# Optimization experiments

Measured on AMD Instinct MI355X. Metric: run time of the kernel, lower is better.

Reference implementation:

```python
import jax, jax.numpy as jnp
import numpy as np
import math

# Model dims (see shape_source)
N_EMBD = 2048
QK_H = 128      # per-head qk dim
V_H = 128       # per-head v dim
Q_DIM = N_EMBD                 # 2048 -> 16 query heads
N_HEAD = Q_DIM // QK_H         # 16
KV_HEAD = N_HEAD // 4          # 4 (GQA)
K_DIM = KV_HEAD * QK_H         # 512
V_DIM = KV_HEAD * V_H          # 512
D_KV = K_DIM + V_DIM           # 1024, S6 channel dim
D_STATE = 16                   # S6 state size
DT_RANK = math.ceil(D_KV / 16) # 'auto' -> 64
WINDOW = 512
B, T = 1, 4096


def setup_inputs() -> dict:
    key = jax.random.key(0)
    ks = jax.random.split(key, 8)
    x = jax.random.normal(ks[0], (B, T, N_EMBD), jnp.float32)
    W_attn = jax.random.normal(ks[1], (Q_DIM + K_DIM + V_DIM, N_EMBD), jnp.float32) * 0.02
    # S6 params (canonical Mamba S6 init: A = -exp(A_log), A_log = log(1..N))
    A_log = jnp.log(jnp.arange(1, D_STATE + 1, dtype=jnp.float32))[None, :] * jnp.ones((D_KV, 1), jnp.float32)
    x_proj_w = jax.random.normal(ks[2], (DT_RANK + 2 * D_STATE, D_KV), jnp.float32) * 0.02
    dt_proj_w = jax.random.normal(ks[3], (D_KV, DT_RANK), jnp.float32) * 0.02
    dt_proj_b = jax.random.normal(ks[4], (D_KV,), jnp.float32) * 0.1
    D_param = jnp.ones((D_KV,), jnp.float32)
    W_o = jax.random.normal(ks[5], (N_EMBD, Q_DIM), jnp.float32) * 0.02
    return dict(x=x, W_attn=W_attn, A_log=A_log, x_proj_w=x_proj_w,
                dt_proj_w=dt_proj_w, dt_proj_b=dt_proj_b, D_param=D_param,
                W_o=W_o, window_size=WINDOW)


def s6_scan(u, A_log, x_proj_w, dt_proj_w, dt_proj_b, D_param):
    """Canonical S6 selective scan. u: (B, T, D) -> (B, T, D)."""
    Bb, Tt, D = u.shape
    N = A_log.shape[1]
    dt_rank = dt_proj_w.shape[1]
    x_dbl = jnp.einsum('btd,ed->bte', u, x_proj_w)          # (B,T,dt_rank+2N)
    dt, Bm, Cm = jnp.split(x_dbl, [dt_rank, dt_rank + N], axis=-1)
    delta = jax.nn.softplus(jnp.einsum('btr,dr->btd', dt, dt_proj_w) + dt_proj_b)  # (B,T,D)
    A = -jnp.exp(A_log)                                      # (D,N), negative
    dA = jnp.exp(delta[..., None] * A)                       # (B,T,D,N)
    dBu = delta[..., None] * Bm[:, :, None, :] * u[..., None]  # (B,T,D,N)

    def step(h, inp):
        dA_t, dBu_t, C_t = inp
        h = dA_t * h + dBu_t                                 # (B,D,N)
        y = jnp.einsum('bdn,bn->bd', h, C_t)
        return h, y

    h0 = jnp.zeros((Bb, D, N), u.dtype)
    _, ys = jax.lax.scan(step, h0,
                         (dA.transpose(1, 0, 2, 3), dBu.transpose(1, 0, 2, 3), Cm.transpose(1, 0, 2)))
    y = ys.transpose(1, 0, 2)                                # (B,T,D)
    return y + D_param * u


def sliding_window_attn(q, k, v, window, scale):
    """Causal sliding-window attention; query i attends to j in [i-(window-1), i].
    q: (B,T,H,dh), k/v: (B,T,Hk,dh). Blockwise with one look-back block."""
    Bb, Tt, H, dh = q.shape
    Hk = k.shape[2]
    G = H // Hk
    k = jnp.repeat(k, G, axis=2)
    v = jnp.repeat(v, G, axis=2)
    W = window
    nb = Tt // W
    # (B,H,nb,W,dh)
    qb = q.reshape(Bb, nb, W, H, dh).transpose(0, 3, 1, 2, 4)
    kb = k.reshape(Bb, nb, W, H, dh).transpose(0, 3, 1, 2, 4)
    vb = v.reshape(Bb, nb, W, H, dh).transpose(0, 3, 1, 2, 4)
    # previous block (zeros for first block)
    kprev = jnp.pad(kb, ((0, 0), (0, 0), (1, 0), (0, 0), (0, 0)))[:, :, :nb]
    vprev = jnp.pad(vb, ((0, 0), (0, 0), (1, 0), (0, 0), (0, 0)))[:, :, :nb]
    k2 = jnp.concatenate([kprev, kb], axis=3)                # (B,H,nb,2W,dh)
    v2 = jnp.concatenate([vprev, vb], axis=3)
    scores = jnp.einsum('bhwid,bhwjd->bhwij', qb * scale, k2)  # (B,H,nb,W,2W)
    i = jnp.arange(W)[:, None]
    j = jnp.arange(2 * W)[None, :]
    rel = i + W - j                                          # absolute i - j
    base_mask = (rel >= 0) & (rel <= W - 1)                  # causal & within window
    blk = jnp.arange(nb)[:, None, None]
    valid = base_mask[None] & ((j[None] >= W) | (blk > 0))   # first block: no look-back
    neg = jnp.finfo(jnp.float32).max
    scores = jnp.where(valid[None, None], scores, -neg)
    attn = jax.nn.softmax(scores.astype(jnp.float32), axis=-1).astype(q.dtype)
    out = jnp.einsum('bhwij,bhwjd->bhwid', attn, v2)         # (B,H,nb,W,dh)
    return out.transpose(0, 2, 3, 1, 4).reshape(Bb, Tt, H, dh)


def reference(x, W_attn, A_log, x_proj_w, dt_proj_w, dt_proj_b, D_param, W_o, window_size):
    Bb, Tt, C = x.shape
    qkv = jnp.einsum('btc,oc->bto', x, W_attn)
    q = qkv[..., :Q_DIM]
    kv = qkv[..., Q_DIM:]
    kv = s6_scan(kv, A_log, x_proj_w, dt_proj_w, dt_proj_b, D_param)
    k = kv[..., :K_DIM]
    v = kv[..., K_DIM:]
    q = q.reshape(Bb, Tt, N_HEAD, QK_H)
    k = k.reshape(Bb, Tt, KV_HEAD, QK_H)
    v = v.reshape(Bb, Tt, KV_HEAD, V_H)
    scale = 1.0 / math.sqrt(QK_H)
    y = sliding_window_attn(q, k, v, window_size, scale)     # (B,T,H,v_h)
    y = y.reshape(Bb, Tt, -1)
    return jnp.einsum('bto,no->btn', y, W_o)
```

## Files before the change

### kernel.cpp

```cpp
#include <hip/hip_runtime.h>
#include <hip/hip_bf16.h>

typedef __hip_bfloat16 bf16;
typedef __attribute__((ext_vector_type(8))) short bf16x8;
typedef __attribute__((ext_vector_type(4))) float f32x4;

#define T_SEQ 4096
#define NEMBD 2048
#define QKVD  3072
#define QDIM  2048
#define DKV   1024
#define KDIM  512
#define NH    16
#define DH    128
#define NST   16
#define DTR   64
#define WIN   512
#define NCHUNK 64
#define CLEN   64

__device__ inline float bf2f(bf16 x) { return __bfloat162float(x); }

struct F8 { float v[8]; };

__device__ inline F8 load_b8(const bf16* p) {
  union { uint4 q; unsigned short s[8]; } u;
  u.q = *reinterpret_cast<const uint4*>(p);
  F8 r;
#pragma unroll
  for (int i = 0; i < 8; i++) r.v[i] = __uint_as_float((unsigned)u.s[i] << 16);
  return r;
}

__device__ inline F8 load8(const void* base, size_t idx, int f32flag) {
  if (f32flag) {
    const float4* p = reinterpret_cast<const float4*>((const float*)base + idx);
    float4 a = p[0], b = p[1];
    F8 r;
    r.v[0]=a.x; r.v[1]=a.y; r.v[2]=a.z; r.v[3]=a.w;
    r.v[4]=b.x; r.v[5]=b.y; r.v[6]=b.z; r.v[7]=b.w;
    return r;
  }
  return load_b8((const bf16*)base + idx);
}

__device__ inline float load1(const void* base, size_t idx, int f32flag) {
  return f32flag ? ((const float*)base)[idx] : bf2f(((const bf16*)base)[idx]);
}

__device__ inline unsigned short f2b_bits(float f) {
  bf16 h = __float2bfloat16(f);
  union { bf16 h; unsigned short u; } c; c.h = h; return c.u;
}

__device__ inline ushort4 pack4(float a, float b, float c, float d) {
  ushort4 r; r.x = f2b_bits(a); r.y = f2b_bits(b); r.z = f2b_bits(c); r.w = f2b_bits(d);
  return r;
}

__device__ inline void gld_lds16(const void* g, void* l) {
  __builtin_amdgcn_global_load_lds(
      (const __attribute__((address_space(1))) unsigned int*)g,
      (__attribute__((address_space(3))) unsigned int*)l, 16, 0, 0);
}

__global__ void detect_dtype(const unsigned short* __restrict__ x, int* __restrict__ flag) {
  if (threadIdx.x == 0 && blockIdx.x == 0) {
    int c = 0;
    for (int i = 0; i < 128; i++) {
      float v = __uint_as_float((unsigned)x[i] << 16);
      float a = fabsf(v);
      if (a >= 1e-8f && a <= 1e4f) c++;
    }
    flag[0] = (c >= 120) ? 0 : 1;
  }
}

__global__ __launch_bounds__(256) void cvt_bf16(
    const void* __restrict__ in, const int* __restrict__ dflag,
    unsigned short* __restrict__ out, int n8)
{
  int i = blockIdx.x * 256 + threadIdx.x;
  if (i >= n8) return;
  const int f = dflag[0];
  F8 v = load8(in, (size_t)i * 8, f);
  ushort4* o = (ushort4*)(out + (size_t)i * 8);
  o[0] = pack4(v.v[0], v.v[1], v.v[2], v.v[3]);
  o[1] = pack4(v.v[4], v.v[5], v.v[6], v.v[7]);
}

__global__ __launch_bounds__(512, 2) void gemm_wide(
    const unsigned short* __restrict__ A, const unsigned short* __restrict__ B,
    int M, int N, int K, int mode,
    bf16* __restrict__ oq, bf16* __restrict__ ou, float* __restrict__ oc)
{
  __shared__ unsigned short lds[2][384 * 64];
  const int tid = threadIdx.x;
  const int wave = tid >> 6, lane = tid & 63;
  const int quad = lane >> 4, l16 = lane & 15;
  const int wm = wave >> 2, wn = wave & 3;
  const int bm = blockIdx.y * 128, bn = blockIdx.x * 256;

  const int lrow = lane >> 3;
  const int lslot = (lane & 7) ^ lrow;
  const unsigned short* Abase = A + (size_t)(bm + wave * 8 + lrow) * K + lslot * 8;
  const unsigned short* Bbase = B + (size_t)(bn + wave * 8 + lrow) * K + lslot * 8;

  const int x7 = l16 & 7;
  const int s0 = ((0 + quad) ^ x7) * 8;
  const int s1 = ((4 + quad) ^ x7) * 8;
  const int arow0 = (wm * 64 + l16) * 64;
  const int brow0 = (128 + wn * 64 + l16) * 64;

  f32x4 acc[4][4];
#pragma unroll
  for (int i = 0; i < 4; i++)
#pragma unroll
    for (int j = 0; j < 4; j++) acc[i][j] = f32x4{0.f, 0.f, 0.f, 0.f};

  const int NT = K >> 6;

  gld_lds16(Abase,                          &lds[0][(0   + wave * 8) * 64]);
  gld_lds16(Abase + (size_t)64 * K,         &lds[0][(64  + wave * 8) * 64]);
  gld_lds16(Bbase,                          &lds[0][(128 + wave * 8) * 64]);
  gld_lds16(Bbase + (size_t)64 * K,         &lds[0][(192 + wave * 8) * 64]);
  gld_lds16(Bbase + (size_t)128 * K,        &lds[0][(256 + wave * 8) * 64]);
  gld_lds16(Bbase + (size_t)192 * K,        &lds[0][(320 + wave * 8) * 64]);
  gld_lds16(Bbase + 64,                     &lds[1][(128 + wave * 8) * 64]);
  gld_lds16(Bbase + (size_t)64 * K + 64,    &lds[1][(192 + wave * 8) * 64]);
  gld_lds16(Bbase + (size_t)128 * K + 64,   &lds[1][(256 + wave * 8) * 64]);
  gld_lds16(Bbase + (size_t)192 * K + 64,   &lds[1][(320 + wave * 8) * 64]);
  asm volatile("s_waitcnt vmcnt(4)" ::: "memory");
  __builtin_amdgcn_sched_barrier(0);
  __builtin_amdgcn_s_barrier();

#define MM(m, n) \
  acc[m][n] = __builtin_amdgcn_mfma_f32_16x16x32_bf16(aF[m][0], bF[n][0], acc[m][n], 0, 0, 0); \
  acc[m][n] = __builtin_amdgcn_mfma_f32_16x16x32_bf16(aF[m][1], bF[n][1], acc[m][n], 0, 0, 0);

  for (int g = 0; g < NT; ++g) {
    const unsigned short* L = lds[g & 1];
    unsigned short* Ln = lds[(g & 1) ^ 1];
    const bool stA = (g + 1) < NT;
    const bool stB = (g + 2) < NT;
    const size_t kA = (size_t)(g + 1) * 64;
    const size_t kB = (size_t)(g + 2) * 64;

    bf16x8 aF[4][2], bF[4][2];

    aF[0][0] = *(const bf16x8*)&L[arow0 +    0 + s0];
    aF[0][1] = *(const bf16x8*)&L[arow0 +    0 + s1];
    aF[1][0] = *(const bf16x8*)&L[arow0 + 1024 + s0];
    aF[1][1] = *(const bf16x8*)&L[arow0 + 1024 + s1];
    bF[0][0] = *(const bf16x8*)&L[brow0 +    0 + s0];
    bF[0][1] = *(const bf16x8*)&L[brow0 +    0 + s1];
    bF[1][0] = *(const bf16x8*)&L[brow0 + 1024 + s0];
    bF[1][1] = *(const bf16x8*)&L[brow0 + 1024 + s1];
    if (stA) gld_lds16(Abase + kA, &Ln[(0 + wave * 8) * 64]);
    __builtin_amdgcn_s_barrier();
    __builtin_amdgcn_s_setprio(1);
    MM(0,0); MM(0,1); MM(1,0); MM(1,1);
    __builtin_amdgcn_s_setprio(0);
    __builtin_amdgcn_s_barrier();

    bF[2][0] = *(const bf16x8*)&L[brow0 + 2048 + s0];
    bF[2][1] = *(const bf16x8*)&L[brow0 + 2048 + s1];
    bF[3][0] = *(const bf16x8*)&L[brow0 + 3072 + s0];
    bF[3][1] = *(const bf16x8*)&L[brow0 + 3072 + s1];
    if (stA) gld_lds16(Abase + (size_t)64 * K + kA, &Ln[(64 + wave * 8) * 64]);
    __builtin_amdgcn_s_barrier();
    __builtin_amdgcn_s_setprio(1);
    MM(0,2); MM(0,3); MM(1,2); MM(1,3);
    __builtin_amdgcn_s_setprio(0);
    __builtin_amdgcn_s_barrier();

    aF[2][0] = *(const bf16x8*)&L[arow0 + 2048 + s0];
    aF[2][1] = *(const bf16x8*)&L[arow0 + 2048 + s1];
    aF[3][0] = *(const bf16x8*)&L[arow0 + 3072 + s0];
    aF[3][1] = *(const bf16x8*)&L[arow0 + 3072 + s1];
    if (stB) {
      gld_lds16(Bbase + kB,                  (unsigned short*)&L[(128 + wave * 8) * 64]);
      gld_lds16(Bbase + (size_t)64 * K + kB, (unsigned short*)&L[(192 + wave * 8) * 64]);
    }
    __builtin_amdgcn_s_barrier();
    __builtin_amdgcn_s_setprio(1);
    MM(2,0); MM(2,1); MM(3,0); MM(3,1);
    __builtin_amdgcn_s_setprio(0);
    __builtin_amdgcn_s_barrier();

    if (stB) {
      gld_lds16(Bbase + (size_t)128 * K + kB, (unsigned short*)&L[(256 + wave * 8) * 64]);
      gld_lds16(Bbase + (size_t)192 * K + kB, (unsigned short*)&L[(320 + wave * 8) * 64]);
    }
    __builtin_amdgcn_s_barrier();
    __builtin_amdgcn_s_setprio(1);
    MM(2,2); MM(2,3); MM(3,2); MM(3,3);
    __builtin_amdgcn_s_setprio(0);
    if (stB) { asm volatile("s_waitcnt vmcnt(4)" ::: "memory"); }
    else     { asm volatile("s_waitcnt vmcnt(0)" ::: "memory"); }
    __builtin_amdgcn_sched_barrier(0);
    __builtin_amdgcn_s_barrier();
  }
#undef MM

#pragma unroll
  for (int m = 0; m < 4; m++)
#pragma unroll
    for (int n = 0; n < 4; n++) {
      int gm0 = bm + wm * 64 + m * 16 + quad * 4;
      int gn  = bn + wn * 64 + n * 16 + l16;
#pragma unroll
      for (int r = 0; r < 4; r++) {
        int gm = gm0 + r;
        float v = acc[m][n][r];
        if (mode == 0) {
          if (gn < QDIM) oq[(size_t)gm * QDIM + gn] = __float2bfloat16(v);
          else           ou[(size_t)gm * DKV + (gn - QDIM)] = __float2bfloat16(v);
        } else {
          oc[(size_t)gm * N + gn] = v;
        }
      }
    }
}

__global__ __launch_bounds__(256) void xdbl_mfma(
    const bf16* __restrict__ u, const unsigned short* __restrict__ xpw_bf,
    float* __restrict__ xd)
{
  __shared__ unsigned short Us[64 * 32];
  __shared__ unsigned short Ws[96 * 32];
  const int tid = threadIdx.x;
  const int wave = tid >> 6, lane = tid & 63;
  const int quad = lane >> 4, l16 = lane & 15;
  const int t0 = blockIdx.x * 64;
  const unsigned short* ub = (const unsigned short*)u;

  f32x4 acc[6];
#pragma unroll
  for (int j = 0; j < 6; j++) acc[j] = f32x4{0.f, 0.f, 0.f, 0.f};

  const int urow = tid >> 2, ucol = (tid & 3) * 8;
  const int wrow0 = tid >> 2, wcol0 = (tid & 3) * 8;
  const int wrow1 = (256 + tid) >> 2;

  uint4 upre = *(const uint4*)(ub + (size_t)(t0 + urow) * DKV + ucol);
  uint4 wpre0 = *(const uint4*)(xpw_bf + (size_t)wrow0 * DKV + wcol0);
  uint4 wpre1 = (tid < 128) ? *(const uint4*)(xpw_bf + (size_t)wrow1 * DKV + wcol0)
                            : uint4{0, 0, 0, 0};

  for (int k0 = 0; k0 < DKV; k0 += 32) {
    __syncthreads();
    *(uint4*)&Us[urow * 32 + ucol] = upre;
    *(uint4*)&Ws[wrow0 * 32 + wcol0] = wpre0;
    if (tid < 128) *(uint4*)&Ws[wrow1 * 32 + wcol0] = wpre1;
    __syncthreads();

    int kn = (k0 + 32 < DKV) ? (k0 + 32) : k0;
    upre  = *(const uint4*)(ub + (size_t)(t0 + urow) * DKV + kn + ucol);
    wpre0 = *(const uint4*)(xpw_bf + (size_t)wrow0 * DKV + kn + wcol0);
    if (tid < 128) wpre1 = *(const uint4*)(xpw_bf + (size_t)wrow1 * DKV + kn + wcol0);

    bf16x8 a = *(const bf16x8*)&Us[(wave * 16 + l16) * 32 + quad * 8];
#pragma unroll
    for (int j = 0; j < 6; j++) {
      bf16x8 b = *(const bf16x8*)&Ws[(j * 16 + l16) * 32 + quad * 8];
      acc[j] = __builtin_amdgcn_mfma_f32_16x16x32_bf16(a, b, acc[j], 0, 0, 0);
    }
  }

#pragma unroll
  for (int j = 0; j < 6; j++)
#pragma unroll
    for (int r = 0; r < 4; r++) {
      int t = t0 + wave * 16 + quad * 4 + r;
      xd[(size_t)t * 96 + j * 16 + l16] = acc[j][r];
    }
}

__global__ __launch_bounds__(256) void delta_mfma(
    const float* __restrict__ xd, const unsigned short* __restrict__ dtw_bf,
    const void* __restrict__ dtb, const int* __restrict__ dflag,
    bf16* __restrict__ delta)
{
  __shared__ unsigned short Xs[64 * 72];
  __shared__ unsigned short Ws[128 * 72];
  const int tid = threadIdx.x;
  const int wave = tid >> 6, lane = tid & 63;
  const int quad = lane >> 4, l16 = lane & 15;
  const int t0 = blockIdx.y * 64, d0 = blockIdx.x * 128;

  for (int e = tid; e < 64 * 8; e += 256) {
    int row = e >> 3, c8 = (e & 7) * 8;
    const float* p = xd + (size_t)(t0 + row) * 96 + c8;
    float4 a = *(const float4*)p, b = *(const float4*)(p + 4);
    *(ushort4*)&Xs[row * 72 + c8]     = pack4(a.x, a.y, a.z, a.w);
    *(ushort4*)&Xs[row * 72 + c8 + 4] = pack4(b.x, b.y, b.z, b.w);
  }
  for (int e = tid; e < 128 * 8; e += 256) {
    int row = e >> 3, c8 = (e & 7) * 8;
    *(uint4*)&Ws[row * 72 + c8] = *(const uint4*)(dtw_bf + (size_t)(d0 + row) * DTR + c8);
  }
  __syncthreads();

  bf16x8 a0 = *(const bf16x8*)&Xs[(wave * 16 + l16) * 72 + quad * 8];
  bf16x8 a1 = *(const bf16x8*)&Xs[(wave * 16 + l16) * 72 + 32 + quad * 8];

  f32x4 acc[8];
#pragma unroll
  for (int j = 0; j < 8; j++) {
    bf16x8 b0 = *(const bf16x8*)&Ws[(j * 16 + l16) * 72 + quad * 8];
    bf16x8 b1 = *(const bf16x8*)&Ws[(j * 16 + l16) * 72 + 32 + quad * 8];
    acc[j] = __builtin_amdgcn_mfma_f32_16x16x32_bf16(a0, b0, f32x4{0.f, 0.f, 0.f, 0.f}, 0, 0, 0);
    acc[j] = __builtin_amdgcn_mfma_f32_16x16x32_bf16(a1, b1, acc[j], 0, 0, 0);
  }

  const int f = dflag[0];
#pragma unroll
  for (int j = 0; j < 8; j++) {
    int d = d0 + j * 16 + l16;
    float bias = load1(dtb, d, f);
#pragma unroll
    for (int r = 0; r < 4; r++) {
      int t = t0 + wave * 16 + quad * 4 + r;
      float v = acc[j][r] + bias;
      float sp = fmaxf(v, 0.f) + log1pf(expf(-fabsf(v)));
      delta[(size_t)t * DKV + d] = __float2bfloat16(sp);
    }
  }
}

__global__ __launch_bounds__(256) void scan_pass1(
    const bf16* __restrict__ delta, const bf16* __restrict__ u,
    const float* __restrict__ xd, const void* __restrict__ A_log,
    const int* __restrict__ dflag, float* __restrict__ Pb, float* __restrict__ Hl)
{
  const int gid = blockIdx.x * 256 + threadIdx.x;
  const int c = gid >> 14;
  const int r = gid & 16383;
  const int d = r >> 4, n = r & 15;
  const int f = dflag[0];
  const float A = -expf(load1(A_log, d * NST + n, f));
  float p = 1.f, h = 0.f;
  const int t0 = c * CLEN;
  for (int tt = 0; tt < CLEN; tt++) {
    int t = t0 + tt;
    float dl = bf2f(delta[(size_t)t * DKV + d]);
    float uu = bf2f(u[(size_t)t * DKV + d]);
    float bm = xd[(size_t)t * 96 + DTR + n];
    float a = expf(dl * A);
    h = a * h + dl * bm * uu;
    p *= a;
  }
  Pb[gid] = p;
  Hl[gid] = h;
}

__global__ __launch_bounds__(256) void scan_combine(
    float* __restrict__ Pb, const float* __restrict__ Hl)
{
  const int idx = blockIdx.x * 256 + threadIdx.x;
  float run = 0.f;
  for (int c = 0; c < NCHUNK; c++) {
    size_t off = (size_t)c * 16384 + idx;
    float p = Pb[off], hl = Hl[off];
    Pb[off] = run;
    run = p * run + hl;
  }
}

__global__ __launch_bounds__(256) void scan_pass2(
    const bf16* __restrict__ delta, bf16* __restrict__ u,
    const float* __restrict__ xd, const void* __restrict__ A_log,
    const void* __restrict__ Dp, const int* __restrict__ dflag,
    const float* __restrict__ Hin)
{
  const int gid = blockIdx.x * 256 + threadIdx.x;
  const int c = gid >> 14;
  const int r = gid & 16383;
  const int d = r >> 4, n = r & 15;
  const int f = dflag[0];
  const float A = -expf(load1(A_log, d * NST + n, f));
  const float dpar = load1(Dp, d, f);
  float h = Hin[gid];
  const int t0 = c * CLEN;
  for (int tt = 0; tt < CLEN; tt++) {
    int t = t0 + tt;
    float dl = bf2f(delta[(size_t)t * DKV + d]);
    float uu = bf2f(u[(size_t)t * DKV + d]);
    float bm = xd[(size_t)t * 96 + DTR + n];
    float cm = xd[(size_t)t * 96 + DTR + NST + n];
    float a = expf(dl * A);
    h = a * h + dl * bm * uu;
    float part = h * cm;
    part += __shfl_xor(part, 1);
    part += __shfl_xor(part, 2);
    part += __shfl_xor(part, 4);
    part += __shfl_xor(part, 8);
    if (n == 0) u[(size_t)t * DKV + d] = __float2bfloat16(part + dpar * uu);
  }
}

__global__ __launch_bounds__(256) void vtrans(
    const bf16* __restrict__ kv, unsigned short* __restrict__ vt)
{
  __shared__ float tile[64][68];
  const int tt0 = blockIdx.x * 64, d0 = blockIdx.y * 64;
  const int tid = threadIdx.x;
  for (int e = tid; e < 64 * 8; e += 256) {
    int row = e >> 3, c8 = (e & 7) * 8;
    F8 v = load_b8(kv + (size_t)(tt0 + row) * DKV + KDIM + d0 + c8);
#pragma unroll
    for (int j = 0; j < 8; j++) tile[row][c8 + j] = v.v[j];
  }
  __syncthreads();
  for (int e = tid; e < 64 * 8; e += 256) {
    int dd = e >> 3, t8 = (e & 7) * 8;
    float vv[8];
#pragma unroll
    for (int j = 0; j < 8; j++) vv[j] = tile[t8 + j][dd];
    ushort4* o = (ushort4*)(vt + (size_t)(d0 + dd) * T_SEQ + tt0 + t8);
    o[0] = pack4(vv[0], vv[1], vv[2], vv[3]);
    o[1] = pack4(vv[4], vv[5], vv[6], vv[7]);
  }
}

__global__ __launch_bounds__(256, 4) void attn_mfma(
    const bf16* __restrict__ q, const bf16* __restrict__ kv,
    const unsigned short* __restrict__ vt, bf16* __restrict__ y)
{
  __shared__ unsigned short Ks[32 * 136];
  __shared__ unsigned short Vts[128 * 40];
  __shared__ unsigned short Ps[4][16 * 40];
  const int tid = threadIdx.x;
  const int wave = tid >> 6, lane = tid & 63;
  const int quad = lane >> 4, l16 = lane & 15;
  const int qt = blockIdx.x, h = blockIdx.y, kvh = h >> 2;
  const int t0 = qt * 64;
  const float scale = 0.088388347648318447f;

  bf16x8 af[4];
#pragma unroll
  for (int s = 0; s < 4; s++)
    af[s] = *(const bf16x8*)(q + (size_t)(t0 + wave * 16 + l16) * QDIM
                             + h * DH + s * 32 + quad * 8);

  const int krow = tid >> 4, kc8 = (tid & 15) * 8;
  const int vrow = tid >> 2, vc8 = (tid & 3) * 8;
  const bf16* kgp = kv + (size_t)kvh * DH;
  const unsigned short* vgp = vt + (size_t)(kvh * DH) * T_SEQ;

  float m_r[4], l_p[4];
  f32x4 O[8];
#pragma unroll
  for (int r = 0; r < 4; r++) { m_r[r] = -1e30f; l_p[r] = 0.f; }
#pragma unroll
  for (int dt = 0; dt < 8; dt++) O[dt] = f32x4{0.f, 0.f, 0.f, 0.f};

  const int kb_start = (t0 > WIN - 1) ? ((t0 - (WIN - 1)) >> 5) : 0;
  const int kb_end = (t0 + 63) >> 5;

  uint4 kp0, kp1, vp0, vp1;
  {
    const int kb = kb_start;
    kp0 = *(const uint4*)(kgp + (size_t)(kb * 32 + krow) * DKV + kc8);
    kp1 = *(const uint4*)(kgp + (size_t)(kb * 32 + 16 + krow) * DKV + kc8);
    vp0 = *(const uint4*)(vgp + (size_t)vrow * T_SEQ + kb * 32 + vc8);
    vp1 = *(const uint4*)(vgp + (size_t)(vrow + 64) * T_SEQ + kb * 32 + vc8);
  }

  for (int kb = kb_start; kb <= kb_end; kb++) {
    __syncthreads();
    *(uint4*)&Ks[krow * 136 + kc8]        = kp0;
    *(uint4*)&Ks[(krow + 16) * 136 + kc8] = kp1;
    *(uint4*)&Vts[vrow * 40 + vc8]        = vp0;
    *(uint4*)&Vts[(vrow + 64) * 40 + vc8] = vp1;
    __syncthreads();

    if (kb < kb_end) {
      const int kn = kb + 1;
      kp0 = *(const uint4*)(kgp + (size_t)(kn * 32 + krow) * DKV + kc8);
      kp1 = *(const uint4*)(kgp + (size_t)(kn * 32 + 16 + krow) * DKV + kc8);
      vp0 = *(const uint4*)(vgp + (size_t)vrow * T_SEQ + kn * 32 + vc8);
      vp1 = *(const uint4*)(vgp + (size_t)(vrow + 64) * T_SEQ + kn * 32 + vc8);
    }

    f32x4 S0 = f32x4{0.f, 0.f, 0.f, 0.f}, S1 = f32x4{0.f, 0.f, 0.f, 0.f};
#pragma unroll
    for (int s = 0; s < 4; s++) {
      bf16x8 b0 = *(const bf16x8*)&Ks[(l16) * 136 + s * 32 + quad * 8];
      bf16x8 b1 = *(const bf16x8*)&Ks[(16 + l16) * 136 + s * 32 + quad * 8];
      S0 = __builtin_amdgcn_mfma_f32_16x16x32_bf16(af[s], b0, S0, 0, 0, 0);
      S1 = __builtin_amdgcn_mfma_f32_16x16x32_bf16(af[s], b1, S1, 0, 0, 0);
    }

    const int ka0 = kb * 32 + l16;
    const int ka1 = ka0 + 16;
    const bool full = (kb * 32 >= t0 + 63 - (WIN - 1)) && (kb * 32 + 31 <= t0);

    float v0r[4], v1r[4];
    bool x0r[4], x1r[4];
    bool ok = true;
#pragma unroll
    for (int r = 0; r < 4; r++) {
      int qa = t0 + wave * 16 + quad * 4 + r;
      float v0 = S0[r] * scale, v1 = S1[r] * scale;
      bool x0 = true, x1 = true;
      if (!full) {
        x0 = (ka0 <= qa) && (ka0 > qa - WIN);
        x1 = (ka1 <= qa) && (ka1 > qa - WIN);
        if (!x0) v0 = -1e30f;
        if (!x1) v1 = -1e30f;
      }
      v0r[r] = v0; v1r[r] = v1; x0r[r] = x0; x1r[r] = x1;
      ok = ok && (fmaxf(v0, v1) <= m_r[r] + 8.f);
    }

    if (!__all((int)ok)) {
#pragma unroll
      for (int r = 0; r < 4; r++) {
        float rm = fmaxf(v0r[r], v1r[r]);
        rm = fmaxf(rm, __shfl_xor(rm, 1));
        rm = fmaxf(rm, __shfl_xor(rm, 2));
        rm = fmaxf(rm, __shfl_xor(rm, 4));
        rm = fmaxf(rm, __shfl_xor(rm, 8));
        float mnew = fmaxf(m_r[r], rm);
        float al = __expf(m_r[r] - mnew);
        m_r[r] = mnew;
        l_p[r] *= al;
#pragma unroll
        for (int dt = 0; dt < 8; dt++) O[dt][r] *= al;
      }
    }

#pragma unroll
    for (int r = 0; r < 4; r++) {
      float p0 = x0r[r] ? __expf(v0r[r] - m_r[r]) : 0.f;
      float p1 = x1r[r] ? __expf(v1r[r] - m_r[r]) : 0.f;
      l_p[r] += p0 + p1;
      Ps[wave][(quad * 4 + r) * 40 + l16]      = f2b_bits(p0);
      Ps[wave][(quad * 4 + r) * 40 + 16 + l16] = f2b_bits(p1);
    }

    bf16x8 pa = *(const bf16x8*)&Ps[wave][l16 * 40 + quad * 8];
#pragma unroll
    for (int dt = 0; dt < 8; dt++) {
      bf16x8 b = *(const bf16x8*)&Vts[(dt * 16 + l16) * 40 + quad * 8];
      O[dt] = __builtin_amdgcn_mfma_f32_16x16x32_bf16(pa, b, O[dt], 0, 0, 0);
    }
  }

  float inv[4];
#pragma unroll
  for (int r = 0; r < 4; r++) {
    float l = l_p[r];
    l += __shfl_xor(l, 1);
    l += __shfl_xor(l, 2);
    l += __shfl_xor(l, 4);
    l += __shfl_xor(l, 8);
    inv[r] = 1.f / l;
  }
#pragma unroll
  for (int dt = 0; dt < 8; dt++)
#pragma unroll
    for (int r = 0; r < 4; r++) {
      int row = t0 + wave * 16 + quad * 4 + r;
      y[(size_t)row * QDIM + h * DH + dt * 16 + l16] = __float2bfloat16(O[dt][r] * inv[r]);
    }
}

extern "C" void kernel_launch(void* const* d_in, const int* in_sizes, int n_in,
                              void* d_out, int out_size, void* d_ws, size_t ws_size,
                              hipStream_t stream)
{
  const void* x      = d_in[0];
  const void* W_attn = d_in[1];
  const void* A_log  = d_in[2];
  const void* xpw    = d_in[3];
  const void* dtw    = d_in[4];
  const void* dtb    = d_in[5];
  const void* Dp     = d_in[6];
  const void* W_o    = d_in[7];

  char* ws = (char*)d_ws;
  int*   dflag = (int*)ws;   ws += 256;
  bf16*  u     = (bf16*)ws;  ws += (size_t)T_SEQ * DKV * 2;
  float* xd    = (float*)ws; ws += (size_t)T_SEQ * 96 * 4;
  char*  yreg  = ws;
  bf16*  delta = (bf16*)ws;  ws += (size_t)T_SEQ * DKV * 2;
  float* Pb    = (float*)ws; ws += (size_t)NCHUNK * DKV * NST * 4;
  float* Hl    = (float*)ws; ws += (size_t)NCHUNK * DKV * NST * 4;
  unsigned short* x_bf  = (unsigned short*)ws; ws += (size_t)T_SEQ * NEMBD * 2;
  unsigned short* wa_bf = (unsigned short*)ws; ws += (size_t)QKVD * NEMBD * 2;
  unsigned short* wo_bf = (unsigned short*)ws; ws += (size_t)NEMBD * QDIM * 2;
  unsigned short* vt    = (unsigned short*)ws; ws += (size_t)KDIM * T_SEQ * 2;
  unsigned short* xpw_bf = (unsigned short*)ws; ws += (size_t)96 * DKV * 2;
  unsigned short* dtw_bf = (unsigned short*)ws; ws += (size_t)DKV * DTR * 2;
  bf16*  y     = (bf16*)yreg;

  bf16*  q_bf = (bf16*)d_out;
  float* out  = (float*)d_out;

  detect_dtype<<<1, 64, 0, stream>>>((const unsigned short*)x, dflag);
  cvt_bf16<<<(T_SEQ * NEMBD / 8 + 255) / 256, 256, 0, stream>>>(x, dflag, x_bf, T_SEQ * NEMBD / 8);
  cvt_bf16<<<(QKVD * NEMBD / 8 + 255) / 256, 256, 0, stream>>>(W_attn, dflag, wa_bf, QKVD * NEMBD / 8);
  cvt_bf16<<<(NEMBD * QDIM / 8 + 255) / 256, 256, 0, stream>>>(W_o, dflag, wo_bf, NEMBD * QDIM / 8);
  cvt_bf16<<<(96 * DKV / 8 + 255) / 256, 256, 0, stream>>>(xpw, dflag, xpw_bf, 96 * DKV / 8);
  cvt_bf16<<<(DKV * DTR / 8 + 255) / 256, 256, 0, stream>>>(dtw, dflag, dtw_bf, DKV * DTR / 8);

  gemm_wide<<<dim3(QKVD / 256, T_SEQ / 128), 512, 0, stream>>>(
      x_bf, wa_bf, T_SEQ, QKVD, NEMBD, 0, q_bf, u, nullptr);
  xdbl_mfma<<<T_SEQ / 64, 256, 0, stream>>>(u, xpw_bf, xd);
  delta_mfma<<<dim3(DKV / 128, T_SEQ / 64), 256, 0, stream>>>(xd, dtw_bf, dtb, dflag, delta);
  scan_pass1<<<4096, 256, 0, stream>>>(delta, u, xd, A_log, dflag, Pb, Hl);
  scan_combine<<<64, 256, 0, stream>>>(Pb, Hl);
  scan_pass2<<<4096, 256, 0, stream>>>(delta, u, xd, A_log, Dp, dflag, Pb);
  vtrans<<<dim3(T_SEQ / 64, KDIM / 64), 256, 0, stream>>>(u, vt);
  attn_mfma<<<dim3(T_SEQ / 64, NH), 256, 0, stream>>>(q_bf, u, vt, y);
  gemm_wide<<<dim3(QDIM / 256, T_SEQ / 128), 512, 0, stream>>>(
      (const unsigned short*)y, wo_bf, T_SEQ, QDIM, QDIM, 1, nullptr, nullptr, out);
}
```

Before: 445.7 us.

## Retile wide GEMM to 256x128 with XCD-aware block swizzle and unified prefetch

The GEMM block tile changes from 128x256 to 256x128 with a 4x2 wave layout, and the 2D grid becomes a 1D grid. Block IDs are remapped so consecutive tiles land on the same XCD (8-way chunking), which is meant to improve L2 reuse of shared A/B panels. The pipeline is simplified so both A and B use a uniform two-stage-ahead prefetch into the current buffer, with fewer barriers per k-step. The swizzle assumes the grid size divides evenly by 8, and the new launch bounds and waitcnt counts must match the changed load count.

```diff
diff --git a/kernel.cpp b/kernel.cpp
--- a/kernel.cpp
+++ b/kernel.cpp
@@ -98,8 +98,12 @@
   const int tid = threadIdx.x;
   const int wave = tid >> 6, lane = tid & 63;
   const int quad = lane >> 4, l16 = lane & 15;
-  const int wm = wave >> 2, wn = wave & 3;
-  const int bm = blockIdx.y * 128, bn = blockIdx.x * 256;
+  const int wm = wave >> 1, wn = wave & 1;
+  const int nbx = N >> 7;
+  const int nwg = gridDim.x;
+  const int chunk = nwg >> 3;
+  const int swz = (blockIdx.x & 7) * chunk + (blockIdx.x >> 3);
+  const int bm = (swz / nbx) * 256, bn = (swz % nbx) * 128;
 
   const int lrow = lane >> 3;
   const int lslot = (lane & 7) ^ lrow;
@@ -110,7 +114,7 @@
   const int s0 = ((0 + quad) ^ x7) * 8;
   const int s1 = ((4 + quad) ^ x7) * 8;
   const int arow0 = (wm * 64 + l16) * 64;
-  const int brow0 = (128 + wn * 64 + l16) * 64;
+  const int brow0 = (256 + wn * 64 + l16) * 64;
 
   f32x4 acc[4][4];
 #pragma unroll
@@ -120,17 +124,19 @@
 
   const int NT = K >> 6;
 
-  gld_lds16(Abase,                          &lds[0][(0   + wave * 8) * 64]);
-  gld_lds16(Abase + (size_t)64 * K,         &lds[0][(64  + wave * 8) * 64]);
-  gld_lds16(Bbase,                          &lds[0][(128 + wave * 8) * 64]);
-  gld_lds16(Bbase + (size_t)64 * K,         &lds[0][(192 + wave * 8) * 64]);
-  gld_lds16(Bbase + (size_t)128 * K,        &lds[0][(256 + wave * 8) * 64]);
-  gld_lds16(Bbase + (size_t)192 * K,        &lds[0][(320 + wave * 8) * 64]);
-  gld_lds16(Bbase + 64,                     &lds[1][(128 + wave * 8) * 64]);
-  gld_lds16(Bbase + (size_t)64 * K + 64,    &lds[1][(192 + wave * 8) * 64]);
-  gld_lds16(Bbase + (size_t)128 * K + 64,   &lds[1][(256 + wave * 8) * 64]);
-  gld_lds16(Bbase + (size_t)192 * K + 64,   &lds[1][(320 + wave * 8) * 64]);
-  asm volatile("s_waitcnt vmcnt(4)" ::: "memory");
+#pragma unroll
+  for (int grp = 0; grp < 4; grp++)
+    gld_lds16(Abase + (size_t)grp * 64 * K, &lds[0][(grp * 64 + wave * 8) * 64]);
+#pragma unroll
+  for (int grp = 0; grp < 2; grp++)
+    gld_lds16(Bbase + (size_t)grp * 64 * K, &lds[0][(256 + grp * 64 + wave * 8) * 64]);
+#pragma unroll
+  for (int grp = 0; grp < 4; grp++)
+    gld_lds16(Abase + (size_t)grp * 64 * K + 64, &lds[1][(grp * 64 + wave * 8) * 64]);
+#pragma unroll
+  for (int grp = 0; grp < 2; grp++)
+    gld_lds16(Bbase + (size_t)grp * 64 * K + 64, &lds[1][(256 + grp * 64 + wave * 8) * 64]);
+  asm volatile("s_waitcnt vmcnt(6)" ::: "memory");
   __builtin_amdgcn_sched_barrier(0);
   __builtin_amdgcn_s_barrier();
 
@@ -140,26 +146,30 @@
 
   for (int g = 0; g < NT; ++g) {
     const unsigned short* L = lds[g & 1];
-    unsigned short* Ln = lds[(g & 1) ^ 1];
-    const bool stA = (g + 1) < NT;
-    const bool stB = (g + 2) < NT;
-    const size_t kA = (size_t)(g + 1) * 64;
-    const size_t kB = (size_t)(g + 2) * 64;
+    unsigned short* Lw = (unsigned short*)L;
+    const bool stF = (g + 2) < NT;
+    const size_t kF = (size_t)(g + 2) * 64;
 
     bf16x8 aF[4][2], bF[4][2];
 
-    aF[0][0] = *(const bf16x8*)&L[arow0 +    0 + s0];
-    aF[0][1] = *(const bf16x8*)&L[arow0 +    0 + s1];
-    aF[1][0] = *(const bf16x8*)&L[arow0 + 1024 + s0];
-    aF[1][1] = *(const bf16x8*)&L[arow0 + 1024 + s1];
+#pragma unroll
+    for (int m = 0; m < 4; m++) {
+      aF[m][0] = *(const bf16x8*)&L[arow0 + m * 1024 + s0];
+      aF[m][1] = *(const bf16x8*)&L[arow0 + m * 1024 + s1];
+    }
     bF[0][0] = *(const bf16x8*)&L[brow0 +    0 + s0];
     bF[0][1] = *(const bf16x8*)&L[brow0 +    0 + s1];
     bF[1][0] = *(const bf16x8*)&L[brow0 + 1024 + s0];
     bF[1][1] = *(const bf16x8*)&L[brow0 + 1024 + s1];
-    if (stA) gld_lds16(Abase + kA, &Ln[(0 + wave * 8) * 64]);
     __builtin_amdgcn_s_barrier();
+    if (stF) {
+#pragma unroll
+      for (int grp = 0; grp < 4; grp++)
+        gld_lds16(Abase + (size_t)grp * 64 * K + kF, &Lw[(grp * 64 + wave * 8) * 64]);
+    }
     __builtin_amdgcn_s_setprio(1);
     MM(0,0); MM(0,1); MM(1,0); MM(1,1);
+    MM(2,0); MM(2,1); MM(3,0); MM(3,1);
     __builtin_amdgcn_s_setprio(0);
     __builtin_amdgcn_s_barrier();
 
@@ -167,36 +177,17 @@
     bF[2][1] = *(const bf16x8*)&L[brow0 + 2048 + s1];
     bF[3][0] = *(const bf16x8*)&L[brow0 + 3072 + s0];
     bF[3][1] = *(const bf16x8*)&L[brow0 + 3072 + s1];
-    if (stA) gld_lds16(Abase + (size_t)64 * K + kA, &Ln[(64 + wave * 8) * 64]);
     __builtin_amdgcn_s_barrier();
+    if (stF) {
+#pragma unroll
+      for (int grp = 0; grp < 2; grp++)
+        gld_lds16(Bbase + (size_t)grp * 64 * K + kF, &Lw[(256 + grp * 64 + wave * 8) * 64]);
+    }
     __builtin_amdgcn_s_setprio(1);
     MM(0,2); MM(0,3); MM(1,2); MM(1,3);
-    __builtin_amdgcn_s_setprio(0);
-    __builtin_amdgcn_s_barrier();
-
-    aF[2][0] = *(const bf16x8*)&L[arow0 + 2048 + s0];
-    aF[2][1] = *(const bf16x8*)&L[arow0 + 2048 + s1];
-    aF[3][0] = *(const bf16x8*)&L[arow0 + 3072 + s0];
-    aF[3][1] = *(const bf16x8*)&L[arow0 + 3072 + s1];
-    if (stB) {
-      gld_lds16(Bbase + kB,                  (unsigned short*)&L[(128 + wave * 8) * 64]);
-      gld_lds16(Bbase + (size_t)64 * K + kB, (unsigned short*)&L[(192 + wave * 8) * 64]);
-    }
-    __builtin_amdgcn_s_barrier();
-    __builtin_amdgcn_s_setprio(1);
-    MM(2,0); MM(2,1); MM(3,0); MM(3,1);
-    __builtin_amdgcn_s_setprio(0);
-    __builtin_amdgcn_s_barrier();
-
-    if (stB) {
-      gld_lds16(Bbase + (size_t)128 * K + kB, (unsigned short*)&L[(256 + wave * 8) * 64]);
-      gld_lds16(Bbase + (size_t)192 * K + kB, (unsigned short*)&L[(320 + wave * 8) * 64]);
-    }
-    __builtin_amdgcn_s_barrier();
-    __builtin_amdgcn_s_setprio(1);
     MM(2,2); MM(2,3); MM(3,2); MM(3,3);
     __builtin_amdgcn_s_setprio(0);
-    if (stB) { asm volatile("s_waitcnt vmcnt(4)" ::: "memory"); }
+    if (stF) { asm volatile("s_waitcnt vmcnt(6)" ::: "memory"); }
     else     { asm volatile("s_waitcnt vmcnt(0)" ::: "memory"); }
     __builtin_amdgcn_sched_barrier(0);
     __builtin_amdgcn_s_barrier();
@@ -607,7 +598,7 @@
   cvt_bf16<<<(96 * DKV / 8 + 255) / 256, 256, 0, stream>>>(xpw, dflag, xpw_bf, 96 * DKV / 8);
   cvt_bf16<<<(DKV * DTR / 8 + 255) / 256, 256, 0, stream>>>(dtw, dflag, dtw_bf, DKV * DTR / 8);
 
-  gemm_wide<<<dim3(QKVD / 256, T_SEQ / 128), 512, 0, stream>>>(
+  gemm_wide<<<(T_SEQ / 256) * (QKVD / 128), 512, 0, stream>>>(
       x_bf, wa_bf, T_SEQ, QKVD, NEMBD, 0, q_bf, u, nullptr);
   xdbl_mfma<<<T_SEQ / 64, 256, 0, stream>>>(u, xpw_bf, xd);
   delta_mfma<<<dim3(DKV / 128, T_SEQ / 64), 256, 0, stream>>>(xd, dtw_bf, dtb, dflag, delta);
@@ -616,6 +607,6 @@
   scan_pass2<<<4096, 256, 0, stream>>>(delta, u, xd, A_log, Dp, dflag, Pb);
   vtrans<<<dim3(T_SEQ / 64, KDIM / 64), 256, 0, stream>>>(u, vt);
   attn_mfma<<<dim3(T_SEQ / 64, NH), 256, 0, stream>>>(q_bf, u, vt, y);
-  gemm_wide<<<dim3(QDIM / 256, T_SEQ / 128), 512, 0, stream>>>(
+  gemm_wide<<<(T_SEQ / 256) * (QDIM / 128), 512, 0, stream>>>(
       (const unsigned short*)y, wo_bf, T_SEQ, QDIM, QDIM, 1, nullptr, nullptr, out);
 }
```

New measurement: 438.3 us. No clear change (-1.7%).
